# Kernel optimization log

Measured on AMD Instinct MI355X. Metric: run time of the kernel, lower is better.

## Reference

```python
import jax, jax.numpy as jnp
import numpy as np

N_NODES_PER_GRAPH = 16
N_GRAPHS = 256
D = 512


def _build_graph(n=N_NODES_PER_GRAPH, B=N_GRAPHS):
    # fully-connected directed graph (no self loops) per sample, DGL insertion order
    ii, jj = np.meshgrid(np.arange(n), np.arange(n), indexing='ij')
    m = ii != jj
    s, d = ii[m], jj[m]                     # [n*(n-1)] src-major order
    offs = (np.arange(B) * n)[:, None]
    src = (s[None, :] + offs).reshape(-1)
    dst = (d[None, :] + offs).reshape(-1)
    E_g = n * (n - 1)
    # target->other edges are (0, dst) for dst in 1..n-1 => first n-1 eids of each graph
    t_o_eid = ((np.arange(B) * E_g)[:, None] + np.arange(n - 1)[None, :]).reshape(-1)
    return src.astype(np.int32), dst.astype(np.int32), t_o_eid.astype(np.int32)


def setup_inputs() -> dict:
    key = jax.random.key(0)
    n, B, d = N_NODES_PER_GRAPH, N_GRAPHS, D
    N = n * B
    src, dst, t_o_eid = _build_graph(n, B)
    E = src.shape[0]
    ks = jax.random.split(key, 6)
    sc = 0.02
    return {
        'visual_feat': jax.random.normal(ks[0], (N, d), jnp.float32),
        'spatial_feat': jax.random.normal(ks[1], (E, d), jnp.float32),
        'W_edge': jax.random.normal(ks[2], (3 * d, d), jnp.float32) * sc,
        'b_edge': jnp.zeros((d,), jnp.float32),
        'W_attn': jax.random.normal(ks[3], (d, 1), jnp.float32) * sc,
        'b_attn': jnp.zeros((1,), jnp.float32),
        'W_node': jax.random.normal(ks[4], (2 * d, d), jnp.float32) * sc,
        'b_node': jnp.zeros((d,), jnp.float32),
        'W_pred': jax.random.normal(ks[5], (3 * d, d), jnp.float32) * sc,
        'b_pred': jnp.zeros((d,), jnp.float32),
        'src': jnp.asarray(src),
        'dst': jnp.asarray(dst),
        't_o_eid': jnp.asarray(t_o_eid),
    }


def reference(visual_feat, spatial_feat, W_edge, b_edge, W_attn, b_attn,
              W_node, b_node, W_pred, b_pred, src, dst, t_o_eid):
    N = visual_feat.shape[0]
    # EdgeApplyModule: gather src/dst node feats, concat with spatial, MLP
    efeat = jnp.concatenate([visual_feat[src], spatial_feat, visual_feat[dst]], axis=1)  # [E,3D]
    e_f = jax.nn.relu(efeat @ W_edge + b_edge)                        # [E,D]
    # EdgeAttentionApplyModule: scalar attention logit per edge
    a = jax.nn.relu(e_f @ W_attn + b_attn)[:, 0]                      # [E]
    # reduce: softmax over incoming-edge mailbox per dst node (segment softmax)
    a_max = jax.ops.segment_max(a, dst, num_segments=N)
    ex = jnp.exp(a - a_max[dst])
    denom = jax.ops.segment_sum(ex, dst, num_segments=N)
    alpha = ex / denom[dst]                                           # [E]
    msg = visual_feat[src] + e_f                                      # old_n_f + e_f
    z_f = jax.ops.segment_sum(alpha[:, None] * msg, dst, num_segments=N)  # [N,D]
    # NodeApplyModule: concat(n_f, z_f) -> MLP
    new_n_f = jax.nn.relu(jnp.concatenate([visual_feat, z_f], axis=1) @ W_node + b_node)
    # interaction predictor on target->other edges
    ts, td = src[t_o_eid], dst[t_o_eid]
    pfeat = jnp.concatenate([new_n_f[ts], spatial_feat[t_o_eid], new_n_f[td]], axis=1)
    pred = jax.nn.relu(pfeat @ W_pred + b_pred)                       # [E_to, D]
    return pred
```

## Files before the change

kernel.cpp:

```cpp
#include <hip/hip_runtime.h>
#include <hip/hip_bf16.h>
#include <stdint.h>

#define BM 128
#define BN 128

typedef __attribute__((ext_vector_type(8))) short bf16x8;
typedef __attribute__((ext_vector_type(4))) float f32x4;
typedef __attribute__((ext_vector_type(4))) uint32_t u32x4;

__device__ __forceinline__ uint32_t pk2(float lo, float hi) {
  union { __hip_bfloat162 h; uint32_t u; } un;
  un.h = __float22bfloat162_rn(make_float2(lo, hi));
  return un.u;
}
__device__ __forceinline__ uint16_t bfc(float f) {
  return (uint16_t)(pk2(f, f) & 0xFFFFu);
}
__device__ __forceinline__ float bf2f(uint16_t s) {
  union { uint32_t u; float f; } v; v.u = ((uint32_t)s) << 16;
  return v.f;
}
__device__ __forceinline__ void gload_lds16(const void* g, void* l) {
  __builtin_amdgcn_global_load_lds((const __attribute__((address_space(1))) void*)g,
                                   (__attribute__((address_space(3))) void*)l, 16, 0, 0);
}
__device__ __forceinline__ int xcd_swz(int d, int n) {
  const int q = n >> 3, r = n & 7, x = d & 7, i = d >> 3;
  return (x < r ? x * (q + 1) : r * (q + 1) + (x - r) * q) + i;
}

enum { E_PLAIN16 = 0, E_EDGE = 1, E_NODE = 2, E_PRED = 3 };

struct GemmArgs {
  const uint16_t* Ab; int lda;
  const float* Af;
  const int* gidx;
  const uint16_t* B0;
  const uint16_t* B1;
  int K;
  int nwg, ncol;
  uint16_t* C16; int ldc;
  const float* bias;
  const float* wattn;
  const int* src; const int* dst; const int* toe;
  const uint16_t* A13;
  const uint16_t* VISB;
  const uint16_t* U13;
  uint16_t* EF;
  float* AATT;
  float* OUT;
};

template <int EPI>
__device__ __forceinline__ void gemm_epilogue(const GemmArgs& g, f32x4 (&acc)[4][2],
                                              int m0, int n0g, int wm, int wn,
                                              int lr, int lg, int vb,
                                              const short* a13s, const short* viss) {
  const int rbase = m0 + wm * 64;
  const int cbase = n0g + wn * 32;
  if constexpr (EPI == E_PLAIN16) {
#pragma unroll
    for (int m = 0; m < 4; ++m)
#pragma unroll
      for (int r = 0; r < 4; ++r) {
        const int row = rbase + m * 16 + lg * 4 + r;
#pragma unroll
        for (int n = 0; n < 2; ++n)
          g.C16[(size_t)row * g.ldc + cbase + n * 16 + lr] = bfc(acc[m][n][r]);
      }
  } else if constexpr (EPI == E_NODE) {
#pragma unroll
    for (int m = 0; m < 4; ++m)
#pragma unroll
      for (int r = 0; r < 4; ++r) {
        const int row = rbase + m * 16 + lg * 4 + r;
#pragma unroll
        for (int n = 0; n < 2; ++n) {
          const int col = cbase + n * 16 + lr;
          g.C16[(size_t)row * g.ldc + col] = bfc(fmaxf(acc[m][n][r] + g.bias[col], 0.f));
        }
      }
  } else if constexpr (EPI == E_EDGE) {
    float bv[2], wv[2]; int lc[2];
#pragma unroll
    for (int n = 0; n < 2; ++n) {
      lc[n] = wn * 32 + n * 16 + lr;
      bv[n] = g.bias[n0g + lc[n]];
      wv[n] = g.wattn[n0g + lc[n]];
    }
#pragma unroll
    for (int m = 0; m < 4; ++m)
#pragma unroll
      for (int r = 0; r < 4; ++r) {
        const int e = rbase + m * 16 + lg * 4 + r;
        const int se = g.src[e] - vb, de = g.dst[e] - vb;
        float rp = 0.f;
#pragma unroll
        for (int n = 0; n < 2; ++n) {
          float v = acc[m][n][r] + bf2f((uint16_t)a13s[se * 256 + lc[n]]) +
                    bf2f((uint16_t)a13s[de * 256 + 128 + lc[n]]) + bv[n];
          v = fmaxf(v, 0.f);
          rp += v * wv[n];
          g.EF[(size_t)e * 512 + n0g + lc[n]] =
              bfc(v + bf2f((uint16_t)viss[se * 128 + lc[n]]));
        }
        for (int d = 1; d < 16; d <<= 1) rp += __shfl_xor(rp, d);
        if (lr == 0) atomicAdd(&g.AATT[e], rp);
      }
  } else {
    float bv[2]; int cols[2];
#pragma unroll
    for (int n = 0; n < 2; ++n) { cols[n] = cbase + n * 16 + lr; bv[n] = g.bias[cols[n]]; }
#pragma unroll
    for (int m = 0; m < 4; ++m)
#pragma unroll
      for (int r = 0; r < 4; ++r) {
        const int row = rbase + m * 16 + lg * 4 + r;
        const int te = g.toe[row];
        const int ts = g.src[te], td = g.dst[te];
        const uint16_t* u1 = g.U13 + (size_t)ts * 1024;
        const uint16_t* u3 = g.U13 + (size_t)td * 1024 + 512;
#pragma unroll
        for (int n = 0; n < 2; ++n) {
          const float v = acc[m][n][r] + bf2f(u1[cols[n]]) + bf2f(u3[cols[n]]) + bv[n];
          g.OUT[(size_t)row * 512 + cols[n]] = fmaxf(v, 0.f);
        }
      }
  }
}

template <int EPI>
__global__ __launch_bounds__(512, 8) void gemm_lds_k(GemmArgs g) {
  __shared__ __align__(16) short As[8192];
  __shared__ __align__(16) short Bs[8192];
  const int tid = threadIdx.x, w = tid >> 6, lane = tid & 63;

  const int sid = xcd_swz(blockIdx.x, g.nwg);
  const int colb = sid % g.ncol, rowb = sid / g.ncol;
  const int m0 = rowb * BM, n0g = colb * BN;

  const uint16_t* Bp = g.B0; int n0 = n0g;
  if (n0g >= 512) { Bp = g.B1; n0 = n0g - 512; }

  const int r1 = tid >> 3;
  const int sc = ((tid & 7) ^ (r1 & 7)) * 8;
  const int d1 = tid * 8;
  const uint16_t* gB1 = Bp + (size_t)(n0 + r1) * g.K + sc;
  const uint16_t* gB2 = gB1 + (size_t)64 * g.K;
  int ga1 = m0 + r1, ga2 = m0 + r1 + 64;
  if (g.gidx) { ga1 = g.gidx[ga1]; ga2 = g.gidx[ga2]; }
  const uint16_t* gA1 = g.Ab + (size_t)ga1 * g.lda + sc;
  const uint16_t* gA2 = g.Ab + (size_t)ga2 * g.lda + sc;

  const int vb = (EPI == E_EDGE) ? (m0 / 240) * 16 : 0;

  const int wm = w >> 2, wn = w & 3;
  const int lr = lane & 15, lg = lane >> 4;
  int aro[2][4], bro[2][2];
#pragma unroll
  for (int h = 0; h < 2; ++h) {
    const int pc = ((h * 4 + lg) ^ (lr & 7)) * 8;
#pragma unroll
    for (int m = 0; m < 4; ++m) aro[h][m] = (wm * 64 + m * 16 + lr) * 64 + pc;
#pragma unroll
    for (int n = 0; n < 2; ++n) bro[h][n] = (wn * 32 + n * 16 + lr) * 64 + pc;
  }

  f32x4 acc[4][2] = {};

  for (int k0 = 0; k0 < g.K; k0 += 64) {
    __syncthreads();
    gload_lds16(gB1 + k0, &Bs[d1]);
    gload_lds16(gB2 + k0, &Bs[d1 + 4096]);
    gload_lds16(gA1 + k0, &As[d1]);
    gload_lds16(gA2 + k0, &As[d1 + 4096]);
    __syncthreads();
#pragma unroll
    for (int h = 0; h < 2; ++h) {
      bf16x8 av[4], bv[2];
#pragma unroll
      for (int m = 0; m < 4; ++m) av[m] = *(const bf16x8*)&As[aro[h][m]];
#pragma unroll
      for (int n = 0; n < 2; ++n) bv[n] = *(const bf16x8*)&Bs[bro[h][n]];
#pragma unroll
      for (int m = 0; m < 4; ++m)
#pragma unroll
        for (int n = 0; n < 2; ++n)
          acc[m][n] = __builtin_amdgcn_mfma_f32_16x16x32_bf16(av[m], bv[n], acc[m][n], 0, 0, 0);
    }
  }

  if constexpr (EPI == E_EDGE) {
    __syncthreads();
#pragma unroll
    for (int rd = 0; rd < 2; ++rd) {
      const int idx = rd * 512 + tid;
      const int node = idx >> 5, chunk = idx & 31;
      const int colg = (chunk < 16) ? (n0g + chunk * 8) : (512 + n0g + (chunk - 16) * 8);
      gload_lds16(g.A13 + (size_t)(vb + node) * 1024 + colg, &As[idx * 8]);
    }
    {
      const int node = tid >> 4, chunk = tid & 15;
      gload_lds16(g.VISB + (size_t)(vb + node) * 512 + n0g + chunk * 8, &Bs[tid * 8]);
    }
    __syncthreads();
  }

  gemm_epilogue<EPI>(g, acc, m0, n0g, wm, wn, lr, lg, vb, As, Bs);
}

template <int EPI>
__global__ __launch_bounds__(512, 8) void gemm_reg_k(GemmArgs g) {
  __shared__ __align__(16) short As[8192];
  __shared__ __align__(16) short Bs[8192];
  const int tid = threadIdx.x, w = tid >> 6, lane = tid & 63;

  const int sid = xcd_swz(blockIdx.x, g.nwg);
  const int colb = sid % g.ncol, rowb = sid / g.ncol;
  const int m0 = rowb * BM, n0g = colb * BN;

  const uint16_t* Bp = g.B0; int n0 = n0g;
  if (n0g >= 512) { Bp = g.B1; n0 = n0g - 512; }

  const int r1 = tid >> 3;
  const int sc = ((tid & 7) ^ (r1 & 7)) * 8;
  const int d1 = tid * 8;
  const uint16_t* gB1 = Bp + (size_t)(n0 + r1) * g.K + sc;
  const uint16_t* gB2 = gB1 + (size_t)64 * g.K;
  int ga1 = m0 + r1, ga2 = m0 + r1 + 64;
  if (g.gidx) { ga1 = g.gidx[ga1]; ga2 = g.gidx[ga2]; }
  const float* fA1 = g.Af + (size_t)ga1 * 512 + sc;
  const float* fA2 = g.Af + (size_t)ga2 * 512 + sc;

  const int vb = (EPI == E_EDGE) ? (m0 / 240) * 16 : 0;

  const int wm = w >> 2, wn = w & 3;
  const int lr = lane & 15, lg = lane >> 4;
  int aro[2][4], bro[2][2];
#pragma unroll
  for (int h = 0; h < 2; ++h) {
    const int pc = ((h * 4 + lg) ^ (lr & 7)) * 8;
#pragma unroll
    for (int m = 0; m < 4; ++m) aro[h][m] = (wm * 64 + m * 16 + lr) * 64 + pc;
#pragma unroll
    for (int n = 0; n < 2; ++n) bro[h][n] = (wn * 32 + n * 16 + lr) * 64 + pc;
  }

  f32x4 acc[4][2] = {};

  for (int k0 = 0; k0 < g.K; k0 += 64) {
    __syncthreads();
    gload_lds16(gB1 + k0, &Bs[d1]);
    gload_lds16(gB2 + k0, &Bs[d1 + 4096]);
    const float4 a0 = *(const float4*)(fA1 + k0);
    const float4 a1 = *(const float4*)(fA1 + k0 + 4);
    const float4 b0 = *(const float4*)(fA2 + k0);
    const float4 b1 = *(const float4*)(fA2 + k0 + 4);
    u32x4 q1, q2;
    q1[0] = pk2(a0.x, a0.y); q1[1] = pk2(a0.z, a0.w);
    q1[2] = pk2(a1.x, a1.y); q1[3] = pk2(a1.z, a1.w);
    q2[0] = pk2(b0.x, b0.y); q2[1] = pk2(b0.z, b0.w);
    q2[2] = pk2(b1.x, b1.y); q2[3] = pk2(b1.z, b1.w);
    *(u32x4*)&As[d1] = q1;
    *(u32x4*)&As[d1 + 4096] = q2;
    __syncthreads();
#pragma unroll
    for (int h = 0; h < 2; ++h) {
      bf16x8 av[4], bv[2];
#pragma unroll
      for (int m = 0; m < 4; ++m) av[m] = *(const bf16x8*)&As[aro[h][m]];
#pragma unroll
      for (int n = 0; n < 2; ++n) bv[n] = *(const bf16x8*)&Bs[bro[h][n]];
#pragma unroll
      for (int m = 0; m < 4; ++m)
#pragma unroll
        for (int n = 0; n < 2; ++n)
          acc[m][n] = __builtin_amdgcn_mfma_f32_16x16x32_bf16(av[m], bv[n], acc[m][n], 0, 0, 0);
    }
  }

  if constexpr (EPI == E_EDGE) {
    __syncthreads();
#pragma unroll
    for (int rd = 0; rd < 2; ++rd) {
      const int idx = rd * 512 + tid;
      const int node = idx >> 5, chunk = idx & 31;
      const int colg = (chunk < 16) ? (n0g + chunk * 8) : (512 + n0g + (chunk - 16) * 8);
      gload_lds16(g.A13 + (size_t)(vb + node) * 1024 + colg, &As[idx * 8]);
    }
    {
      const int node = tid >> 4, chunk = tid & 15;
      gload_lds16(g.VISB + (size_t)(vb + node) * 512 + n0g + chunk * 8, &Bs[tid * 8]);
    }
    __syncthreads();
  }

  gemm_epilogue<EPI>(g, acc, m0, n0g, wm, wn, lr, lg, vb, As, Bs);
}

__global__ __launch_bounds__(256) void prep_k(const float* vis, const float* We,
                                              const float* Wn, const float* Wp,
                                              uint16_t* VISB, uint16_t* NIN,
                                              uint16_t* WT, float* AATT) {
  __shared__ float tile[32][33];
  const int b = blockIdx.x, tid = threadIdx.x;
  if (b < 1024) {
    const int base = (b * 256 + tid) * 8;
    const int row = base >> 9, col = base & 511;
    const float4 f0 = *(const float4*)(vis + base);
    const float4 f1 = *(const float4*)(vis + base + 4);
    u32x4 u;
    u[0] = pk2(f0.x, f0.y); u[1] = pk2(f0.z, f0.w);
    u[2] = pk2(f1.x, f1.y); u[3] = pk2(f1.z, f1.w);
    *(u32x4*)(VISB + base) = u;
    *(u32x4*)(NIN + (size_t)row * 1024 + col) = u;
  } else if (b < 3072) {
    const int zb = b - 1024, z = zb >> 8, rem = zb & 255;
    const float* srcp; uint16_t* dstp; int ldo = 512, koff = 0;
    switch (z) {
      default:
      case 0: srcp = We;          dstp = WT;           break;
      case 1: srcp = We + 262144; dstp = WT + 262144;  break;
      case 2: srcp = We + 524288; dstp = WT + 524288;  break;
      case 3: srcp = Wn;          dstp = WT + 786432;  ldo = 1024; break;
      case 4: srcp = Wn + 262144; dstp = WT + 786432;  ldo = 1024; koff = 512; break;
      case 5: srcp = Wp;          dstp = WT + 1310720; break;
      case 6: srcp = Wp + 262144; dstp = WT + 1572864; break;
      case 7: srcp = Wp + 524288; dstp = WT + 1835008; break;
    }
    const int kb = (rem & 15) * 32, nb = (rem >> 4) * 32;
    const int tx = tid & 31, ty = tid >> 5;
#pragma unroll
    for (int s = 0; s < 4; ++s)
      tile[ty + 8 * s][tx] = srcp[(size_t)(kb + ty + 8 * s) * 512 + nb + tx];
    __syncthreads();
#pragma unroll
    for (int s = 0; s < 4; ++s) {
      const int n = nb + ty + 8 * s, k = kb + tx;
      dstp[(size_t)n * ldo + koff + k] = bfc(tile[tx][ty + 8 * s]);
    }
  } else {
    const int i = (b - 3072) * 1024 + tid * 4;
    float4 z4; z4.x = z4.y = z4.z = z4.w = 0.f;
    *(float4*)(AATT + i) = z4;
  }
}

__global__ __launch_bounds__(256) void node_reduce_k(const float* AATT, const float* battn,
                                                     const uint16_t* MSG, uint16_t* NIN) {
  const int sub = threadIdx.x >> 7;
  const int t = threadIdx.x & 127;
  const int v = blockIdx.x * 2 + sub;
  const int gph = v >> 4, j = v & 15;
  __shared__ float sa_s[2][16];
  __shared__ float alf_s[2][16];
  __shared__ int eids_s[2][16];
  if (t < 15) {
    const int i = (t < j) ? t : t + 1;
    const int off = (j < i) ? j : (j - 1);
    const int eid = gph * 240 + i * 15 + off;
    eids_s[sub][t] = eid;
    sa_s[sub][t] = fmaxf(AATT[eid] + battn[0], 0.f);
  }
  __syncthreads();
  float mx = -1e30f;
#pragma unroll
  for (int i = 0; i < 15; ++i) mx = fmaxf(mx, sa_s[sub][i]);
  float den = 0.f;
#pragma unroll
  for (int i = 0; i < 15; ++i) den += expf(sa_s[sub][i] - mx);
  if (t < 15) alf_s[sub][t] = expf(sa_s[sub][t] - mx) / den;
  __syncthreads();
  const int c = t * 4;
  float z0 = 0.f, z1 = 0.f, z2 = 0.f, z3 = 0.f;
#pragma unroll
  for (int i = 0; i < 15; ++i) {
    const float a = alf_s[sub][i];
    const ushort4 e4 = *(const ushort4*)(MSG + (size_t)eids_s[sub][i] * 512 + c);
    z0 += a * bf2f(e4.x); z1 += a * bf2f(e4.y);
    z2 += a * bf2f(e4.z); z3 += a * bf2f(e4.w);
  }
  ushort4 o;
  o.x = bfc(z0); o.y = bfc(z1); o.z = bfc(z2); o.w = bfc(z3);
  *(ushort4*)(NIN + (size_t)v * 1024 + 512 + c) = o;
}

extern "C" void kernel_launch(void* const* d_in, const int* in_sizes, int n_in,
                              void* d_out, int out_size, void* d_ws, size_t ws_size,
                              hipStream_t stream) {
  const float* visual = (const float*)d_in[0];
  const float* spatial = (const float*)d_in[1];
  const float* W_edge = (const float*)d_in[2];
  const float* b_edge = (const float*)d_in[3];
  const float* W_attn = (const float*)d_in[4];
  const float* b_attn = (const float*)d_in[5];
  const float* W_node = (const float*)d_in[6];
  const float* b_node = (const float*)d_in[7];
  const float* W_pred = (const float*)d_in[8];
  const float* b_pred = (const float*)d_in[9];
  const int* src = (const int*)d_in[10];
  const int* dst = (const int*)d_in[11];
  const int* toe = (const int*)d_in[12];
  float* out = (float*)d_out;

  char* ws = (char*)d_ws;
  uint16_t* WT = (uint16_t*)ws;
  uint16_t* VISB = (uint16_t*)(ws + 4194304);
  uint16_t* NIN = (uint16_t*)(ws + 8388608);
  uint16_t* A13b = (uint16_t*)(ws + 16777216);
  uint16_t* EF = (uint16_t*)(ws + 25165824);
  float* AATT = (float*)(ws + 88080384);
  uint16_t* U13b = A13b;
  uint16_t* NNF = EF;

  prep_k<<<3132, 256, 0, stream>>>(visual, W_edge, W_node, W_pred, VISB, NIN, WT, AATT);

  const dim3 blk(512);
  {
    GemmArgs a = {};
    a.Ab = VISB; a.lda = 512; a.B0 = WT; a.B1 = WT + 524288; a.K = 512;
    a.nwg = 256; a.ncol = 8;
    a.C16 = A13b; a.ldc = 1024;
    gemm_lds_k<E_PLAIN16><<<256, blk, 0, stream>>>(a);
  }
  {
    GemmArgs a = {};
    a.Af = spatial; a.B0 = WT + 262144; a.K = 512;
    a.nwg = 1920; a.ncol = 4;
    a.bias = b_edge; a.wattn = W_attn;
    a.src = src; a.dst = dst; a.A13 = A13b; a.VISB = VISB; a.EF = EF; a.AATT = AATT;
    gemm_reg_k<E_EDGE><<<1920, blk, 0, stream>>>(a);
  }
  node_reduce_k<<<2048, 256, 0, stream>>>(AATT, b_attn, EF, NIN);
  {
    GemmArgs a = {};
    a.Ab = NIN; a.lda = 1024; a.B0 = WT + 786432; a.K = 1024;
    a.nwg = 128; a.ncol = 4;
    a.bias = b_node; a.C16 = NNF; a.ldc = 512;
    gemm_lds_k<E_NODE><<<128, blk, 0, stream>>>(a);
  }
  {
    GemmArgs a = {};
    a.Ab = NNF; a.lda = 512; a.B0 = WT + 1310720; a.B1 = WT + 1835008; a.K = 512;
    a.nwg = 256; a.ncol = 8;
    a.C16 = U13b; a.ldc = 1024;
    gemm_lds_k<E_PLAIN16><<<256, blk, 0, stream>>>(a);
  }
  {
    GemmArgs a = {};
    a.Af = spatial; a.gidx = toe; a.B0 = WT + 1572864; a.K = 512;
    a.nwg = 120; a.ncol = 4;
    a.bias = b_pred; a.toe = toe; a.src = src; a.dst = dst; a.U13 = U13b; a.OUT = out;
    gemm_reg_k<E_PRED><<<120, blk, 0, stream>>>(a);
  }
  (void)in_sizes; (void)n_in; (void)out_size; (void)ws_size;
}
```

Measured before the change: 178.6 us.

## Widen register-path GEMM tile to 128x256 so fp32 spatial A loads once

Changes the register-converting GEMM kernel, used by the edge and predictor stages, from a 128x128 to a 128x256 output tile. Each block now covers half the output columns, so the large fp32 spatial feature rows are read and converted to bf16 half as often. The edge and predictor epilogues move into the kernel and are widened to four column fragments, and the staged node tiles are resized to fit the larger LDS buffers. In exchange, accumulator registers double, the occupancy hint drops from 8 to 4, and launches shrink to 960 and 60 blocks, which may leave compute units idle for the predictor stage.

```diff
diff --git a/kernel.cpp b/kernel.cpp
--- a/kernel.cpp
+++ b/kernel.cpp
@@ -3,7 +3,6 @@
 #include <stdint.h>
 
 #define BM 128
-#define BN 128
 
 typedef __attribute__((ext_vector_type(8))) short bf16x8;
 typedef __attribute__((ext_vector_type(4))) float f32x4;
@@ -53,10 +52,9 @@
 };
 
 template <int EPI>
-__device__ __forceinline__ void gemm_epilogue(const GemmArgs& g, f32x4 (&acc)[4][2],
-                                              int m0, int n0g, int wm, int wn,
-                                              int lr, int lg, int vb,
-                                              const short* a13s, const short* viss) {
+__device__ __forceinline__ void gemm_epilogue128(const GemmArgs& g, f32x4 (&acc)[4][2],
+                                                 int m0, int n0g, int wm, int wn,
+                                                 int lr, int lg) {
   const int rbase = m0 + wm * 64;
   const int cbase = n0g + wn * 32;
   if constexpr (EPI == E_PLAIN16) {
@@ -69,7 +67,7 @@
         for (int n = 0; n < 2; ++n)
           g.C16[(size_t)row * g.ldc + cbase + n * 16 + lr] = bfc(acc[m][n][r]);
       }
-  } else if constexpr (EPI == E_NODE) {
+  } else {
 #pragma unroll
     for (int m = 0; m < 4; ++m)
 #pragma unroll
@@ -81,52 +79,6 @@
           g.C16[(size_t)row * g.ldc + col] = bfc(fmaxf(acc[m][n][r] + g.bias[col], 0.f));
         }
       }
-  } else if constexpr (EPI == E_EDGE) {
-    float bv[2], wv[2]; int lc[2];
-#pragma unroll
-    for (int n = 0; n < 2; ++n) {
-      lc[n] = wn * 32 + n * 16 + lr;
-      bv[n] = g.bias[n0g + lc[n]];
-      wv[n] = g.wattn[n0g + lc[n]];
-    }
-#pragma unroll
-    for (int m = 0; m < 4; ++m)
-#pragma unroll
-      for (int r = 0; r < 4; ++r) {
-        const int e = rbase + m * 16 + lg * 4 + r;
-        const int se = g.src[e] - vb, de = g.dst[e] - vb;
-        float rp = 0.f;
-#pragma unroll
-        for (int n = 0; n < 2; ++n) {
-          float v = acc[m][n][r] + bf2f((uint16_t)a13s[se * 256 + lc[n]]) +
-                    bf2f((uint16_t)a13s[de * 256 + 128 + lc[n]]) + bv[n];
-          v = fmaxf(v, 0.f);
-          rp += v * wv[n];
-          g.EF[(size_t)e * 512 + n0g + lc[n]] =
-              bfc(v + bf2f((uint16_t)viss[se * 128 + lc[n]]));
-        }
-        for (int d = 1; d < 16; d <<= 1) rp += __shfl_xor(rp, d);
-        if (lr == 0) atomicAdd(&g.AATT[e], rp);
-      }
-  } else {
-    float bv[2]; int cols[2];
-#pragma unroll
-    for (int n = 0; n < 2; ++n) { cols[n] = cbase + n * 16 + lr; bv[n] = g.bias[cols[n]]; }
-#pragma unroll
-    for (int m = 0; m < 4; ++m)
-#pragma unroll
-      for (int r = 0; r < 4; ++r) {
-        const int row = rbase + m * 16 + lg * 4 + r;
-        const int te = g.toe[row];
-        const int ts = g.src[te], td = g.dst[te];
-        const uint16_t* u1 = g.U13 + (size_t)ts * 1024;
-        const uint16_t* u3 = g.U13 + (size_t)td * 1024 + 512;
-#pragma unroll
-        for (int n = 0; n < 2; ++n) {
-          const float v = acc[m][n][r] + bf2f(u1[cols[n]]) + bf2f(u3[cols[n]]) + bv[n];
-          g.OUT[(size_t)row * 512 + cols[n]] = fmaxf(v, 0.f);
-        }
-      }
   }
 }
 
@@ -138,7 +90,7 @@
 
   const int sid = xcd_swz(blockIdx.x, g.nwg);
   const int colb = sid % g.ncol, rowb = sid / g.ncol;
-  const int m0 = rowb * BM, n0g = colb * BN;
+  const int m0 = rowb * BM, n0g = colb * 128;
 
   const uint16_t* Bp = g.B0; int n0 = n0g;
   if (n0g >= 512) { Bp = g.B1; n0 = n0g - 512; }
@@ -153,8 +105,6 @@
   const uint16_t* gA1 = g.Ab + (size_t)ga1 * g.lda + sc;
   const uint16_t* gA2 = g.Ab + (size_t)ga2 * g.lda + sc;
 
-  const int vb = (EPI == E_EDGE) ? (m0 / 240) * 16 : 0;
-
   const int wm = w >> 2, wn = w & 3;
   const int lr = lane & 15, lg = lane >> 4;
   int aro[2][4], bro[2][2];
@@ -191,43 +141,27 @@
     }
   }
 
-  if constexpr (EPI == E_EDGE) {
-    __syncthreads();
-#pragma unroll
-    for (int rd = 0; rd < 2; ++rd) {
-      const int idx = rd * 512 + tid;
-      const int node = idx >> 5, chunk = idx & 31;
-      const int colg = (chunk < 16) ? (n0g + chunk * 8) : (512 + n0g + (chunk - 16) * 8);
-      gload_lds16(g.A13 + (size_t)(vb + node) * 1024 + colg, &As[idx * 8]);
-    }
-    {
-      const int node = tid >> 4, chunk = tid & 15;
-      gload_lds16(g.VISB + (size_t)(vb + node) * 512 + n0g + chunk * 8, &Bs[tid * 8]);
-    }
-    __syncthreads();
-  }
-
-  gemm_epilogue<EPI>(g, acc, m0, n0g, wm, wn, lr, lg, vb, As, Bs);
+  gemm_epilogue128<EPI>(g, acc, m0, n0g, wm, wn, lr, lg);
 }
 
 template <int EPI>
-__global__ __launch_bounds__(512, 8) void gemm_reg_k(GemmArgs g) {
+__global__ __launch_bounds__(512, 4) void gemm_reg_k(GemmArgs g) {
   __shared__ __align__(16) short As[8192];
-  __shared__ __align__(16) short Bs[8192];
+  __shared__ __align__(16) short Bs[16384];
   const int tid = threadIdx.x, w = tid >> 6, lane = tid & 63;
 
   const int sid = xcd_swz(blockIdx.x, g.nwg);
   const int colb = sid % g.ncol, rowb = sid / g.ncol;
-  const int m0 = rowb * BM, n0g = colb * BN;
-
-  const uint16_t* Bp = g.B0; int n0 = n0g;
-  if (n0g >= 512) { Bp = g.B1; n0 = n0g - 512; }
+  const int m0 = rowb * BM, n0g = colb * 256;
+
+  const uint16_t* Bp = g.B0;
 
   const int r1 = tid >> 3;
   const int sc = ((tid & 7) ^ (r1 & 7)) * 8;
   const int d1 = tid * 8;
-  const uint16_t* gB1 = Bp + (size_t)(n0 + r1) * g.K + sc;
-  const uint16_t* gB2 = gB1 + (size_t)64 * g.K;
+  const uint16_t* gB[4];
+#pragma unroll
+  for (int s = 0; s < 4; ++s) gB[s] = Bp + (size_t)(n0g + r1 + s * 64) * g.K + sc;
   int ga1 = m0 + r1, ga2 = m0 + r1 + 64;
   if (g.gidx) { ga1 = g.gidx[ga1]; ga2 = g.gidx[ga2]; }
   const float* fA1 = g.Af + (size_t)ga1 * 512 + sc;
@@ -237,22 +171,22 @@
 
   const int wm = w >> 2, wn = w & 3;
   const int lr = lane & 15, lg = lane >> 4;
-  int aro[2][4], bro[2][2];
+  int aro[2][4], bro[2][4];
 #pragma unroll
   for (int h = 0; h < 2; ++h) {
     const int pc = ((h * 4 + lg) ^ (lr & 7)) * 8;
 #pragma unroll
     for (int m = 0; m < 4; ++m) aro[h][m] = (wm * 64 + m * 16 + lr) * 64 + pc;
 #pragma unroll
-    for (int n = 0; n < 2; ++n) bro[h][n] = (wn * 32 + n * 16 + lr) * 64 + pc;
-  }
-
-  f32x4 acc[4][2] = {};
+    for (int n = 0; n < 4; ++n) bro[h][n] = (wn * 64 + n * 16 + lr) * 64 + pc;
+  }
+
+  f32x4 acc[4][4] = {};
 
   for (int k0 = 0; k0 < g.K; k0 += 64) {
     __syncthreads();
-    gload_lds16(gB1 + k0, &Bs[d1]);
-    gload_lds16(gB2 + k0, &Bs[d1 + 4096]);
+#pragma unroll
+    for (int s = 0; s < 4; ++s) gload_lds16(gB[s] + k0, &Bs[d1 + s * 4096]);
     const float4 a0 = *(const float4*)(fA1 + k0);
     const float4 a1 = *(const float4*)(fA1 + k0 + 4);
     const float4 b0 = *(const float4*)(fA2 + k0);
@@ -267,36 +201,87 @@
     __syncthreads();
 #pragma unroll
     for (int h = 0; h < 2; ++h) {
-      bf16x8 av[4], bv[2];
+      bf16x8 av[4], bv[4];
 #pragma unroll
       for (int m = 0; m < 4; ++m) av[m] = *(const bf16x8*)&As[aro[h][m]];
 #pragma unroll
-      for (int n = 0; n < 2; ++n) bv[n] = *(const bf16x8*)&Bs[bro[h][n]];
+      for (int n = 0; n < 4; ++n) bv[n] = *(const bf16x8*)&Bs[bro[h][n]];
 #pragma unroll
       for (int m = 0; m < 4; ++m)
 #pragma unroll
-        for (int n = 0; n < 2; ++n)
+        for (int n = 0; n < 4; ++n)
           acc[m][n] = __builtin_amdgcn_mfma_f32_16x16x32_bf16(av[m], bv[n], acc[m][n], 0, 0, 0);
     }
   }
 
+  const int rbase = m0 + wm * 64;
+
   if constexpr (EPI == E_EDGE) {
     __syncthreads();
+#pragma unroll
+    for (int rd = 0; rd < 4; ++rd) {
+      const int idx = rd * 512 + tid;
+      const int node = idx >> 6, chunk = idx & 63;
+      const int colg = (chunk < 32) ? (n0g + chunk * 8) : (512 + n0g + (chunk - 32) * 8);
+      gload_lds16(g.A13 + (size_t)(vb + node) * 1024 + colg, &Bs[idx * 8]);
+    }
 #pragma unroll
     for (int rd = 0; rd < 2; ++rd) {
       const int idx = rd * 512 + tid;
       const int node = idx >> 5, chunk = idx & 31;
-      const int colg = (chunk < 16) ? (n0g + chunk * 8) : (512 + n0g + (chunk - 16) * 8);
-      gload_lds16(g.A13 + (size_t)(vb + node) * 1024 + colg, &As[idx * 8]);
-    }
-    {
-      const int node = tid >> 4, chunk = tid & 15;
-      gload_lds16(g.VISB + (size_t)(vb + node) * 512 + n0g + chunk * 8, &Bs[tid * 8]);
-    }
-    __syncthreads();
-  }
-
-  gemm_epilogue<EPI>(g, acc, m0, n0g, wm, wn, lr, lg, vb, As, Bs);
+      gload_lds16(g.VISB + (size_t)(vb + node) * 512 + n0g + chunk * 8, &As[idx * 8]);
+    }
+    __syncthreads();
+
+    float bv[4], wv[4]; int lc[4];
+#pragma unroll
+    for (int n = 0; n < 4; ++n) {
+      lc[n] = wn * 64 + n * 16 + lr;
+      bv[n] = g.bias[n0g + lc[n]];
+      wv[n] = g.wattn[n0g + lc[n]];
+    }
+#pragma unroll
+    for (int m = 0; m < 4; ++m)
+#pragma unroll
+      for (int r = 0; r < 4; ++r) {
+        const int e = rbase + m * 16 + lg * 4 + r;
+        const int se = g.src[e] - vb, de = g.dst[e] - vb;
+        float rp = 0.f;
+#pragma unroll
+        for (int n = 0; n < 4; ++n) {
+          float v = acc[m][n][r] + bf2f((uint16_t)Bs[se * 512 + lc[n]]) +
+                    bf2f((uint16_t)Bs[de * 512 + 256 + lc[n]]) + bv[n];
+          v = fmaxf(v, 0.f);
+          rp += v * wv[n];
+          g.EF[(size_t)e * 512 + n0g + lc[n]] =
+              bfc(v + bf2f((uint16_t)As[se * 256 + lc[n]]));
+        }
+        for (int d = 1; d < 16; d <<= 1) rp += __shfl_xor(rp, d);
+        if (lr == 0) atomicAdd(&g.AATT[e], rp);
+      }
+  } else {
+    float bv[4]; int cols[4];
+#pragma unroll
+    for (int n = 0; n < 4; ++n) {
+      cols[n] = n0g + wn * 64 + n * 16 + lr;
+      bv[n] = g.bias[cols[n]];
+    }
+#pragma unroll
+    for (int m = 0; m < 4; ++m)
+#pragma unroll
+      for (int r = 0; r < 4; ++r) {
+        const int row = rbase + m * 16 + lg * 4 + r;
+        const int te = g.toe[row];
+        const int ts = g.src[te], td = g.dst[te];
+        const uint16_t* u1 = g.U13 + (size_t)ts * 1024;
+        const uint16_t* u3 = g.U13 + (size_t)td * 1024 + 512;
+#pragma unroll
+        for (int n = 0; n < 4; ++n) {
+          const float v = acc[m][n][r] + bf2f(u1[cols[n]]) + bf2f(u3[cols[n]]) + bv[n];
+          g.OUT[(size_t)row * 512 + cols[n]] = fmaxf(v, 0.f);
+        }
+      }
+  }
 }
 
 __global__ __launch_bounds__(256) void prep_k(const float* vis, const float* We,
@@ -427,10 +412,10 @@
   {
     GemmArgs a = {};
     a.Af = spatial; a.B0 = WT + 262144; a.K = 512;
-    a.nwg = 1920; a.ncol = 4;
+    a.nwg = 960; a.ncol = 2;
     a.bias = b_edge; a.wattn = W_attn;
     a.src = src; a.dst = dst; a.A13 = A13b; a.VISB = VISB; a.EF = EF; a.AATT = AATT;
-    gemm_reg_k<E_EDGE><<<1920, blk, 0, stream>>>(a);
+    gemm_reg_k<E_EDGE><<<960, blk, 0, stream>>>(a);
   }
   node_reduce_k<<<2048, 256, 0, stream>>>(AATT, b_attn, EF, NIN);
   {
@@ -450,9 +435,9 @@
   {
     GemmArgs a = {};
     a.Af = spatial; a.gidx = toe; a.B0 = WT + 1572864; a.K = 512;
-    a.nwg = 120; a.ncol = 4;
+    a.nwg = 60; a.ncol = 2;
     a.bias = b_pred; a.toe = toe; a.src = src; a.dst = dst; a.U13 = U13b; a.OUT = out;
-    gemm_reg_k<E_PRED><<<120, blk, 0, stream>>>(a);
+    gemm_reg_k<E_PRED><<<60, blk, 0, stream>>>(a);
   }
   (void)in_sizes; (void)n_in; (void)out_size; (void)ws_size;
 }
```

Result: faster. 146.4 us, median of 2 (-18.1%).
